# Kernel tuning notes

Hardware: AMD Instinct MI355X
Metric: run time of the kernel (lower is better)

## Reference

```python
import jax, jax.numpy as jnp
import numpy as np
from jax import lax

# Pool config mirroring SfmPool(window_shape=3, strides=2, padding='SAME', channel_axis=-1, T=1.0)
# on an NHWC input -> window (1,3,3,1), strides (1,2,2,1).
WS = (1, 3, 3, 1)
ST = (1, 2, 2, 1)
PAD = "SAME"
T = 1.0


def _window_wise_max(x):
    """Grad trick from the original module: for each element, sum over all windows
    covering it of that window's max (identical math, including overlap counts)."""
    ones = jnp.ones_like(x)

    def f(o, xx):
        sum_pooled = lax.reduce_window(o, 0.0, lax.add, WS, ST, PAD)
        max_pooled = lax.reduce_window(xx, -jnp.inf, lax.max, WS, ST, PAD)
        return jnp.sum(sum_pooled * max_pooled)

    return jax.grad(f)(ones, x)


def setup_inputs() -> dict:
    key = jax.random.key(0)
    value = jax.random.normal(key, (32, 128, 128, 192), dtype=jnp.float32)
    return {"value": value}


def reference(value):
    t = jnp.asarray(T, dtype=value.dtype)
    tmp_v = value / t
    max_v = _window_wise_max(tmp_v)
    safe_exp = jnp.exp(tmp_v - lax.stop_gradient(max_v))
    numer = value * safe_exp
    pooled_num = lax.reduce_window(numer, 0.0, lax.add, WS, ST, PAD)
    pooled_den = lax.reduce_window(safe_exp, 0.0, lax.add, WS, ST, PAD)
    return pooled_num / pooled_den  # [32, 64, 64, 192]
```

## Files before the change

kernel.cpp:

```cpp
#include <hip/hip_runtime.h>
#include <math.h>


#define B  32
#define H  128
#define W  128
#define C  192
#define OH 64
#define OW 64
#define S  4
#define G  (OH / S)
#define NR (2 * S + 5)
#define NW (S + 2)
#define NCR (2 * S + 1)
#define CB (C * 4)
#define OSTRIDE (OW * C * 4)
#define NEG_INF (-__builtin_inff())

template <bool WAL, bool WAH, bool WQL, bool WQH>
__device__ __forceinline__ float emit1(const float* Mm1, const float* M0,
                                       const float* Mp1, const float* c0,
                                       const float* c1, const float* c2) {
    const float Z00 = (WAL && WQL) ? Mm1[0] : 0.f;
    const float Z01 = WAL ? M0[0] : 0.f;
    const float Z02 = (WAL && WQH) ? Mp1[0] : 0.f;
    const float Z10 = WQL ? Mm1[1] : 0.f;
    const float Z11 = M0[1];
    const float Z12 = WQH ? Mp1[1] : 0.f;
    const float Z20 = (WAH && WQL) ? Mm1[2] : 0.f;
    const float Z21 = WAH ? M0[2] : 0.f;
    const float Z22 = (WAH && WQH) ? Mp1[2] : 0.f;

    const float T0a0 = Z00 + Z01, T0a1 = Z10 + Z11, T0a2 = Z20 + Z21;
    const float T2a0 = Z01 + Z02, T2a1 = Z11 + Z12, T2a2 = Z21 + Z22;

    const float mv00 = T0a0 + T0a1;
    const float mv01 = Z01 + Z11;
    const float mv02 = T2a0 + T2a1;
    const float mv10 = T0a1;
    const float mv11 = Z11;
    const float mv12 = T2a1;
    const float mv20 = T0a1 + T0a2;
    const float mv21 = Z11 + Z21;
    const float mv22 = T2a1 + T2a2;

    float num = 0.f, den = 0.f, v, e;
    v = c0[0]; e = __expf(v - mv00); num = fmaf(v, e, num); den += e;
    v = c1[0]; e = __expf(v - mv01); num = fmaf(v, e, num); den += e;
    v = c0[1]; e = __expf(v - mv10); num = fmaf(v, e, num); den += e;
    v = c1[1]; e = __expf(v - mv11); num = fmaf(v, e, num); den += e;
    if (WQH) {
        v = c2[0]; e = __expf(v - mv02); num = fmaf(v, e, num); den += e;
        v = c2[1]; e = __expf(v - mv12); num = fmaf(v, e, num); den += e;
    }
    if (WAH) {
        v = c0[2]; e = __expf(v - mv20); num = fmaf(v, e, num); den += e;
        v = c1[2]; e = __expf(v - mv21); num = fmaf(v, e, num); den += e;
        if (WQH) {
            v = c2[2]; e = __expf(v - mv22); num = fmaf(v, e, num); den += e;
        }
    }
    return __fdividef(num, den);
}

template <int PAR, int RLO, int RHI, bool WALO, bool WAHI, bool LOADVL,
          bool LOADVR, bool EMIT, bool WQL, bool WQH>
__device__ __forceinline__ void step(const char* __restrict__ sb,
                                     unsigned off[NR], float vmP[NW],
                                     float Mh[2][NW], float CL[2][NCR],
                                     float CR[2][NCR], char* __restrict__ ob,
                                     unsigned& ooff) {
    float vl[NR], vr[NR];
#pragma unroll
    for (int r = 0; r < NR; ++r) {
        const bool rv = (r >= RLO && r <= RHI);
        vl[r] = (LOADVL && rv) ? *(const float*)(sb + off[r]) : NEG_INF;
        vr[r] = (LOADVR && rv) ? *(const float*)(sb + off[r] + CB) : NEG_INF;
    }
    float vmL[NW], vmR[NW], Mp[NW];
#pragma unroll
    for (int w = 0; w < NW; ++w) {
        vmL[w] = fmaxf(fmaxf(vl[2 * w], vl[2 * w + 1]), vl[2 * w + 2]);
        vmR[w] = fmaxf(fmaxf(vr[2 * w], vr[2 * w + 1]), vr[2 * w + 2]);
        Mp[w] = fmaxf(fmaxf(vmP[w], vmL[w]), vmR[w]);
    }
    if (EMIT) {
        {
            float o = emit1<WALO, true, WQL, WQH>(
                &Mh[PAR][0], &Mh[PAR ^ 1][0], &Mp[0],
                &CR[PAR][0], &CL[PAR ^ 1][0], &CR[PAR ^ 1][0]);
            *(float*)(ob + ooff + 0 * OSTRIDE) = o;
        }
        {
            float o = emit1<true, true, WQL, WQH>(
                &Mh[PAR][1], &Mh[PAR ^ 1][1], &Mp[1],
                &CR[PAR][2], &CL[PAR ^ 1][2], &CR[PAR ^ 1][2]);
            *(float*)(ob + ooff + 1 * OSTRIDE) = o;
        }
        {
            float o = emit1<true, true, WQL, WQH>(
                &Mh[PAR][2], &Mh[PAR ^ 1][2], &Mp[2],
                &CR[PAR][4], &CL[PAR ^ 1][4], &CR[PAR ^ 1][4]);
            *(float*)(ob + ooff + 2 * OSTRIDE) = o;
        }
        {
            float o = emit1<true, WAHI, WQL, WQH>(
                &Mh[PAR][3], &Mh[PAR ^ 1][3], &Mp[3],
                &CR[PAR][6], &CL[PAR ^ 1][6], &CR[PAR ^ 1][6]);
            *(float*)(ob + ooff + 3 * OSTRIDE) = o;
        }
        ooff += CB;
    }
#pragma unroll
    for (int w = 0; w < NW; ++w) {
        Mh[PAR][w] = Mp[w];
        vmP[w] = vmR[w];
    }
#pragma unroll
    for (int k = 0; k < NCR; ++k) {
        CL[PAR][k] = vl[k + 2];
        CR[PAR][k] = vr[k + 2];
    }
    if (LOADVL) {
#pragma unroll
        for (int r = 0; r < NR; ++r)
            if (r >= RLO && r <= RHI) off[r] += 2 * CB;
    }
}

template <int RLO, int RHI, bool WALO, bool WAHI, bool FIRST>
__device__ __forceinline__ void sweep(const char* __restrict__ sb,
                                      char* __restrict__ ob, int oh0, int c) {
    constexpr int start = FIRST ? 0 : OW / 2;
    const int j0 = FIRST ? 0 : (2 * start - 2);

    unsigned off[NR];
#pragma unroll
    for (int r = 0; r < NR; ++r) {
        int i = 2 * oh0 - 2 + r;
        if (i < 0) i = 0;
        if (i > H - 1) i = H - 1;
        off[r] = (unsigned)(((i * W + j0) * C + c) * 4);
    }

    float vmP[NW], Mh[2][NW], CL[2][NCR], CR[2][NCR];
    unsigned ooff = (unsigned)(((oh0 * OW + start) * C + c) * 4);

    float v0[NR];
#pragma unroll
    for (int r = 0; r < NR; ++r)
        v0[r] = (r >= RLO && r <= RHI) ? *(const float*)(sb + off[r]) : NEG_INF;

    if (FIRST) {
#pragma unroll
        for (int w = 0; w < NW; ++w) {
            float vm0 = fmaxf(fmaxf(v0[2 * w], v0[2 * w + 1]), v0[2 * w + 2]);
            Mh[1][w] = vm0;
            vmP[w] = vm0;
        }
#pragma unroll
        for (int k = 0; k < NCR; ++k) {
            CL[1][k] = NEG_INF;
            CR[1][k] = v0[k + 2];
        }
    } else {
#pragma unroll
        for (int w = 0; w < NW; ++w)
            vmP[w] = fmaxf(fmaxf(v0[2 * w], v0[2 * w + 1]), v0[2 * w + 2]);
    }
#pragma unroll
    for (int r = 0; r < NR; ++r)
        if (r >= RLO && r <= RHI) off[r] += CB;

    if (!FIRST) {
        step<1, RLO, RHI, WALO, WAHI, true, true, false, true, true>(
            sb, off, vmP, Mh, CL, CR, ob, ooff);
    }
    step<0, RLO, RHI, WALO, WAHI, true, true, false, true, true>(
        sb, off, vmP, Mh, CL, CR, ob, ooff);

    if (FIRST) {
        step<1, RLO, RHI, WALO, WAHI, true, true, true, false, true>(
            sb, off, vmP, Mh, CL, CR, ob, ooff);
#pragma unroll 1
        for (int t = 0; t < 15; ++t) {
            step<0, RLO, RHI, WALO, WAHI, true, true, true, true, true>(
                sb, off, vmP, Mh, CL, CR, ob, ooff);
            step<1, RLO, RHI, WALO, WAHI, true, true, true, true, true>(
                sb, off, vmP, Mh, CL, CR, ob, ooff);
        }
        step<0, RLO, RHI, WALO, WAHI, true, true, true, true, true>(
            sb, off, vmP, Mh, CL, CR, ob, ooff);
    } else {
#pragma unroll 1
        for (int t = 0; t < 15; ++t) {
            step<1, RLO, RHI, WALO, WAHI, true, true, true, true, true>(
                sb, off, vmP, Mh, CL, CR, ob, ooff);
            step<0, RLO, RHI, WALO, WAHI, true, true, true, true, true>(
                sb, off, vmP, Mh, CL, CR, ob, ooff);
        }
        step<1, RLO, RHI, WALO, WAHI, true, false, true, true, true>(
            sb, off, vmP, Mh, CL, CR, ob, ooff);
        step<0, RLO, RHI, WALO, WAHI, false, false, true, true, false>(
            sb, off, vmP, Mh, CL, CR, ob, ooff);
    }
}

__global__ __launch_bounds__(192, 3) void sfmpool_s4_kernel(
    const float* __restrict__ in, float* __restrict__ out) {
    const int c = threadIdx.x;
    const int half = blockIdx.x;
    const int g = blockIdx.y;
    const int b = blockIdx.z;
    const char* sb = (const char*)(in + (size_t)b * (H * W * C));
    char* ob = (char*)(out + (size_t)b * (OH * OW * C));
    const int oh0 = g * S;

    if (g == 0) {
        if (half == 0) sweep<2, 12, false, true, true>(sb, ob, oh0, c);
        else           sweep<2, 12, false, true, false>(sb, ob, oh0, c);
    } else if (g == G - 1) {
        if (half == 0) sweep<0, 9, true, false, true>(sb, ob, oh0, c);
        else           sweep<0, 9, true, false, false>(sb, ob, oh0, c);
    } else {
        if (half == 0) sweep<0, 12, true, true, true>(sb, ob, oh0, c);
        else           sweep<0, 12, true, true, false>(sb, ob, oh0, c);
    }
}

extern "C" void kernel_launch(void* const* d_in, const int* in_sizes, int n_in,
                              void* d_out, int out_size, void* d_ws, size_t ws_size,
                              hipStream_t stream) {
    const float* in = (const float*)d_in[0];
    float* out = (float*)d_out;
    dim3 grid(2, G, B);
    dim3 block(C);
    sfmpool_s4_kernel<<<grid, block, 0, stream>>>(in, out);
}
```

Baseline: 559.4 us.

## Software-pipeline column loads with double-buffered register sets ahead of compute

Splits each sweep step into separate load-issue and compute phases. Two register buffers (A/B) hold the left and right column loads, and each buffer is refilled right after its step is consumed, so global-load latency overlaps the exp/max arithmetic of the other step. It also switches from per-row unsigned offsets to per-row base pointers plus one shared column offset, which cuts the number of address increments. The extra buffers roughly double the live registers for loaded values, which could spill or reduce occupancy under the 192x3 launch bounds.

```diff
diff --git a/kernel.cpp b/kernel.cpp
--- a/kernel.cpp
+++ b/kernel.cpp
@@ -14,6 +14,7 @@
 #define NW (S + 2)
 #define NCR (2 * S + 1)
 #define CB (C * 4)
+#define ROWB (W * C * 4)
 #define OSTRIDE (OW * C * 4)
 #define NEG_INF (-__builtin_inff())
 
@@ -63,19 +64,33 @@
     return __fdividef(num, den);
 }
 
-template <int PAR, int RLO, int RHI, bool WALO, bool WAHI, bool LOADVL,
-          bool LOADVR, bool EMIT, bool WQL, bool WQH>
-__device__ __forceinline__ void step(const char* __restrict__ sb,
-                                     unsigned off[NR], float vmP[NW],
-                                     float Mh[2][NW], float CL[2][NCR],
-                                     float CR[2][NCR], char* __restrict__ ob,
-                                     unsigned& ooff) {
+template <int RLO, int RHI, bool LV, bool LR>
+__device__ __forceinline__ void issue_loads(const char* const rp[NR],
+                                            unsigned voff, float vl[NR],
+                                            float vr[NR]) {
+#pragma unroll
+    for (int r = 0; r < NR; ++r) {
+        if (r >= RLO && r <= RHI) {
+            if (LV) vl[r] = *(const float*)(rp[r] + voff);
+            if (LR) vr[r] = *(const float*)(rp[r] + voff + CB);
+        }
+    }
+}
+
+template <int PAR, int RLO, int RHI, bool VL, bool VR, bool WALO, bool WAHI,
+          bool EMIT, bool WQL, bool WQH>
+__device__ __forceinline__ void compute_step(const float vlr[NR],
+                                             const float vrr[NR], float vmP[NW],
+                                             float Mh[2][NW], float CL[2][NCR],
+                                             float CR[2][NCR],
+                                             char* __restrict__ ob,
+                                             unsigned& ooff) {
     float vl[NR], vr[NR];
 #pragma unroll
     for (int r = 0; r < NR; ++r) {
         const bool rv = (r >= RLO && r <= RHI);
-        vl[r] = (LOADVL && rv) ? *(const float*)(sb + off[r]) : NEG_INF;
-        vr[r] = (LOADVR && rv) ? *(const float*)(sb + off[r] + CB) : NEG_INF;
+        vl[r] = (VL && rv) ? vlr[r] : NEG_INF;
+        vr[r] = (VR && rv) ? vrr[r] : NEG_INF;
     }
     float vmL[NW], vmR[NW], Mp[NW];
 #pragma unroll
@@ -120,11 +135,6 @@
     for (int k = 0; k < NCR; ++k) {
         CL[PAR][k] = vl[k + 2];
         CR[PAR][k] = vr[k + 2];
-    }
-    if (LOADVL) {
-#pragma unroll
-        for (int r = 0; r < NR; ++r)
-            if (r >= RLO && r <= RHI) off[r] += 2 * CB;
     }
 }
 
@@ -134,75 +144,101 @@
     constexpr int start = FIRST ? 0 : OW / 2;
     const int j0 = FIRST ? 0 : (2 * start - 2);
 
-    unsigned off[NR];
+    const char* rp[NR];
 #pragma unroll
     for (int r = 0; r < NR; ++r) {
         int i = 2 * oh0 - 2 + r;
         if (i < 0) i = 0;
         if (i > H - 1) i = H - 1;
-        off[r] = (unsigned)(((i * W + j0) * C + c) * 4);
-    }
+        rp[r] = sb + (size_t)i * ROWB;
+    }
+    unsigned voff = (unsigned)((j0 * C + c) * 4);
+    unsigned ooff = (unsigned)(((oh0 * OW + start) * C + c) * 4);
 
     float vmP[NW], Mh[2][NW], CL[2][NCR], CR[2][NCR];
-    unsigned ooff = (unsigned)(((oh0 * OW + start) * C + c) * 4);
-
-    float v0[NR];
+    float v0[NR], vlA[NR], vrA[NR], vlB[NR], vrB[NR];
+
+    issue_loads<RLO, RHI, true, false>(rp, voff, v0, v0);
+    voff += CB;
+    if (FIRST) {
+        issue_loads<RLO, RHI, true, true>(rp, voff, vlA, vrA); voff += 2 * CB;
+        issue_loads<RLO, RHI, true, true>(rp, voff, vlB, vrB); voff += 2 * CB;
+    } else {
+        issue_loads<RLO, RHI, true, true>(rp, voff, vlB, vrB); voff += 2 * CB;
+        issue_loads<RLO, RHI, true, true>(rp, voff, vlA, vrA); voff += 2 * CB;
+    }
+
+    float v0m[NR];
 #pragma unroll
     for (int r = 0; r < NR; ++r)
-        v0[r] = (r >= RLO && r <= RHI) ? *(const float*)(sb + off[r]) : NEG_INF;
+        v0m[r] = (r >= RLO && r <= RHI) ? v0[r] : NEG_INF;
 
     if (FIRST) {
 #pragma unroll
         for (int w = 0; w < NW; ++w) {
-            float vm0 = fmaxf(fmaxf(v0[2 * w], v0[2 * w + 1]), v0[2 * w + 2]);
+            float vm0 = fmaxf(fmaxf(v0m[2 * w], v0m[2 * w + 1]), v0m[2 * w + 2]);
             Mh[1][w] = vm0;
             vmP[w] = vm0;
         }
 #pragma unroll
         for (int k = 0; k < NCR; ++k) {
             CL[1][k] = NEG_INF;
-            CR[1][k] = v0[k + 2];
+            CR[1][k] = v0m[k + 2];
         }
     } else {
 #pragma unroll
         for (int w = 0; w < NW; ++w)
-            vmP[w] = fmaxf(fmaxf(v0[2 * w], v0[2 * w + 1]), v0[2 * w + 2]);
-    }
-#pragma unroll
-    for (int r = 0; r < NR; ++r)
-        if (r >= RLO && r <= RHI) off[r] += CB;
-
-    if (!FIRST) {
-        step<1, RLO, RHI, WALO, WAHI, true, true, false, true, true>(
-            sb, off, vmP, Mh, CL, CR, ob, ooff);
-    }
-    step<0, RLO, RHI, WALO, WAHI, true, true, false, true, true>(
-        sb, off, vmP, Mh, CL, CR, ob, ooff);
+            vmP[w] = fmaxf(fmaxf(v0m[2 * w], v0m[2 * w + 1]), v0m[2 * w + 2]);
+    }
 
     if (FIRST) {
-        step<1, RLO, RHI, WALO, WAHI, true, true, true, false, true>(
-            sb, off, vmP, Mh, CL, CR, ob, ooff);
+        compute_step<0, RLO, RHI, true, true, WALO, WAHI, false, true, true>(
+            vlA, vrA, vmP, Mh, CL, CR, ob, ooff);
+        issue_loads<RLO, RHI, true, true>(rp, voff, vlA, vrA); voff += 2 * CB;
+        compute_step<1, RLO, RHI, true, true, WALO, WAHI, true, false, true>(
+            vlB, vrB, vmP, Mh, CL, CR, ob, ooff);
+        issue_loads<RLO, RHI, true, true>(rp, voff, vlB, vrB); voff += 2 * CB;
 #pragma unroll 1
-        for (int t = 0; t < 15; ++t) {
-            step<0, RLO, RHI, WALO, WAHI, true, true, true, true, true>(
-                sb, off, vmP, Mh, CL, CR, ob, ooff);
-            step<1, RLO, RHI, WALO, WAHI, true, true, true, true, true>(
-                sb, off, vmP, Mh, CL, CR, ob, ooff);
-        }
-        step<0, RLO, RHI, WALO, WAHI, true, true, true, true, true>(
-            sb, off, vmP, Mh, CL, CR, ob, ooff);
-    } else {
+        for (int t = 0; t < 14; ++t) {
+            compute_step<0, RLO, RHI, true, true, WALO, WAHI, true, true, true>(
+                vlA, vrA, vmP, Mh, CL, CR, ob, ooff);
+            issue_loads<RLO, RHI, true, true>(rp, voff, vlA, vrA); voff += 2 * CB;
+            compute_step<1, RLO, RHI, true, true, WALO, WAHI, true, true, true>(
+                vlB, vrB, vmP, Mh, CL, CR, ob, ooff);
+            issue_loads<RLO, RHI, true, true>(rp, voff, vlB, vrB); voff += 2 * CB;
+        }
+        compute_step<0, RLO, RHI, true, true, WALO, WAHI, true, true, true>(
+            vlA, vrA, vmP, Mh, CL, CR, ob, ooff);
+        issue_loads<RLO, RHI, true, true>(rp, voff, vlA, vrA); voff += 2 * CB;
+        compute_step<1, RLO, RHI, true, true, WALO, WAHI, true, true, true>(
+            vlB, vrB, vmP, Mh, CL, CR, ob, ooff);
+        compute_step<0, RLO, RHI, true, true, WALO, WAHI, true, true, true>(
+            vlA, vrA, vmP, Mh, CL, CR, ob, ooff);
+    } else {
+        compute_step<1, RLO, RHI, true, true, WALO, WAHI, false, true, true>(
+            vlB, vrB, vmP, Mh, CL, CR, ob, ooff);
+        issue_loads<RLO, RHI, true, true>(rp, voff, vlB, vrB); voff += 2 * CB;
+        compute_step<0, RLO, RHI, true, true, WALO, WAHI, false, true, true>(
+            vlA, vrA, vmP, Mh, CL, CR, ob, ooff);
+        issue_loads<RLO, RHI, true, true>(rp, voff, vlA, vrA); voff += 2 * CB;
 #pragma unroll 1
-        for (int t = 0; t < 15; ++t) {
-            step<1, RLO, RHI, WALO, WAHI, true, true, true, true, true>(
-                sb, off, vmP, Mh, CL, CR, ob, ooff);
-            step<0, RLO, RHI, WALO, WAHI, true, true, true, true, true>(
-                sb, off, vmP, Mh, CL, CR, ob, ooff);
-        }
-        step<1, RLO, RHI, WALO, WAHI, true, false, true, true, true>(
-            sb, off, vmP, Mh, CL, CR, ob, ooff);
-        step<0, RLO, RHI, WALO, WAHI, false, false, true, true, false>(
-            sb, off, vmP, Mh, CL, CR, ob, ooff);
+        for (int t = 0; t < 14; ++t) {
+            compute_step<1, RLO, RHI, true, true, WALO, WAHI, true, true, true>(
+                vlB, vrB, vmP, Mh, CL, CR, ob, ooff);
+            issue_loads<RLO, RHI, true, true>(rp, voff, vlB, vrB); voff += 2 * CB;
+            compute_step<0, RLO, RHI, true, true, WALO, WAHI, true, true, true>(
+                vlA, vrA, vmP, Mh, CL, CR, ob, ooff);
+            issue_loads<RLO, RHI, true, true>(rp, voff, vlA, vrA); voff += 2 * CB;
+        }
+        compute_step<1, RLO, RHI, true, true, WALO, WAHI, true, true, true>(
+            vlB, vrB, vmP, Mh, CL, CR, ob, ooff);
+        issue_loads<RLO, RHI, true, false>(rp, voff, vlB, vrB);
+        compute_step<0, RLO, RHI, true, true, WALO, WAHI, true, true, true>(
+            vlA, vrA, vmP, Mh, CL, CR, ob, ooff);
+        compute_step<1, RLO, RHI, true, false, WALO, WAHI, true, true, true>(
+            vlB, vrB, vmP, Mh, CL, CR, ob, ooff);
+        compute_step<0, RLO, RHI, false, false, WALO, WAHI, true, true, false>(
+            vlA, vrA, vmP, Mh, CL, CR, ob, ooff);
     }
 }
 
```

New measurement: 559.8 us. No clear change (+0.1%).
